# Kernel optimization log

Hardware: AMD Instinct MI355X
Metric: run time of the kernel (lower is better)

The kernel has to match this reference:

```python
import jax, jax.numpy as jnp
import numpy as np

N, E = 50000, 800000
IN_F, OUT_F, H = 128, 128, 4
D = OUT_F // H  # head dim
NEG_SLOPE = 0.2
EPS = 1e-12


def setup_inputs() -> dict:
    key = jax.random.key(0)
    ks = jax.random.split(key, 10)
    s = 1.0 / np.sqrt(IN_F)
    return {
        "x": jax.random.normal(ks[0], (N, IN_F), jnp.float32),
        "W_src": jax.random.normal(ks[1], (IN_F, H * D), jnp.float32) * s,
        "b_src": jnp.zeros((H * D,), jnp.float32),
        "W_dst": jax.random.normal(ks[2], (IN_F, H * D), jnp.float32) * s,
        "b_dst": jnp.zeros((H * D,), jnp.float32),
        "attn": jax.random.normal(ks[3], (H, D), jnp.float32) * (1.0 / np.sqrt(D)),
        "out_bias": jnp.zeros((H * D,), jnp.float32),
        "ln_w": jnp.ones((OUT_F,), jnp.float32),
        "ln_b": jnp.zeros((OUT_F,), jnp.float32),
        "src": jax.random.randint(ks[4], (E,), 0, N, jnp.int32),
        "dst": jax.random.randint(ks[5], (E,), 0, N, jnp.int32),
    }


def reference(x, W_src, b_src, W_dst, b_dst, attn, out_bias, ln_w, ln_b, src, dst):
    n = x.shape[0]
    # GATv2Conv (share_weights=False): separate source/dest projections
    fs = (x @ W_src + b_src).reshape(n, H, D)  # [N,H,D]
    fd = (x @ W_dst + b_dst).reshape(n, H, D)
    # per-edge scores: e_ij = attn . leaky_relu(fs[u] + fd[v])
    e = jax.nn.leaky_relu(fs[src] + fd[dst], NEG_SLOPE)  # [E,H,D]
    logits = jnp.einsum("ehd,hd->eh", e, attn)  # [E,H]
    # edge softmax over incoming edges of each dst node
    m = jax.ops.segment_max(logits, dst, num_segments=n)  # [N,H]
    ex = jnp.exp(logits - m[dst])
    denom = jax.ops.segment_sum(ex, dst, num_segments=n)  # [N,H]
    alpha = ex / denom[dst]  # [E,H]
    # aggregate: sum_j alpha_ij * fs[j]
    msg = alpha[:, :, None] * fs[src]  # [E,H,D]
    rst = jax.ops.segment_sum(msg, dst, num_segments=n)  # [N,H,D]
    h = rst.reshape(n, H * D) + out_bias
    # LayerNorm (biased variance, eps inside sqrt)
    u = h.mean(-1, keepdims=True)
    s = jnp.mean((h - u) ** 2, -1, keepdims=True)
    h = (h - u) / jnp.sqrt(s + EPS)
    h = ln_w * h + ln_b
    # activation = elu; dropout p=0 -> identity
    return jax.nn.elu(h)
```

## Files before the change

### kernel.cpp

```cpp
#include <hip/hip_runtime.h>
#include <hip/hip_bf16.h>

constexpr int NF = 128;

using bf16x8 = __attribute__((ext_vector_type(8))) short;
using f32x4v = __attribute__((ext_vector_type(4))) float;

__device__ __forceinline__ unsigned short f2bs(float f) {
    return __builtin_bit_cast(unsigned short, __float2bfloat16(f));
}
__device__ __forceinline__ void unpack8(float4 raw, float* a) {
    unsigned u0 = __float_as_uint(raw.x);
    unsigned u1 = __float_as_uint(raw.y);
    unsigned u2 = __float_as_uint(raw.z);
    unsigned u3 = __float_as_uint(raw.w);
    a[0] = __uint_as_float(u0 << 16);
    a[1] = __uint_as_float(u0 & 0xffff0000u);
    a[2] = __uint_as_float(u1 << 16);
    a[3] = __uint_as_float(u1 & 0xffff0000u);
    a[4] = __uint_as_float(u2 << 16);
    a[5] = __uint_as_float(u2 & 0xffff0000u);
    a[6] = __uint_as_float(u3 << 16);
    a[7] = __uint_as_float(u3 & 0xffff0000u);
}

__global__ void GraphAttnLayer_70196945486348_kernel() {}

__global__ __launch_bounds__(256) void prep_kernel(
    const float* __restrict__ Wsrc, const float* __restrict__ Wdst,
    unsigned short* __restrict__ Wb,
    int* __restrict__ state, int NSB)
{
    int i = blockIdx.x * 256 + threadIdx.x;
    if (i < NSB) state[i] = 0;
    if (i < 256 * NF) {
        int k   = i >> 8;
        int col = i & 255;
        float v = (col < 128) ? Wsrc[k * NF + col] : Wdst[k * NF + (col - 128)];
        Wb[col * NF + k] = f2bs(v);
    }
}

__global__ __launch_bounds__(256) void gemm_hist_kernel(
    const float* __restrict__ x,
    const unsigned short* __restrict__ Wb,
    const float* __restrict__ bsrc, const float* __restrict__ bdst,
    unsigned short* __restrict__ fs,
    float* __restrict__ fd,
    const int* __restrict__ dst,
    int* __restrict__ cntT,
    int N, int E, int C, int B)
{
    __shared__ int lh[256];
    const int t = threadIdx.x;
    if (blockIdx.x < C) {
        lh[t] = 0;
        __syncthreads();
        int e0 = blockIdx.x * 4096;
#pragma unroll
        for (int j = 0; j < 16; ++j) {
            int e = e0 + j * 256 + t;
            if (e < E) atomicAdd(&lh[dst[e] >> 8], 1);
        }
        __syncthreads();
        if (t < B) cntT[t * C + blockIdx.x] = lh[t];
    }

    const int lane = t & 63;
    const int wave = t >> 6;
    const int m_base = blockIdx.x * 32;
    if (m_base >= N) return;
    const int lm = lane & 15;
    const int kq = (lane >> 4) * 8;

    bf16x8 bfrag[4][4];
    float bias[4];
#pragma unroll
    for (int c = 0; c < 4; ++c) {
        int col = wave * 64 + c * 16 + lm;
        bias[c] = (col < 128) ? bsrc[col] : bdst[col - 128];
#pragma unroll
        for (int s = 0; s < 4; ++s)
            bfrag[c][s] = *(const bf16x8*)(Wb + col * NF + s * 32 + kq);
    }

    for (int r = 0; r < 2; ++r) {
        int m0 = m_base + r * 16;
        if (m0 >= N) break;
        int row = m0 + lm;
        if (row >= N) row = N - 1;
        bf16x8 afrag[4];
#pragma unroll
        for (int s = 0; s < 4; ++s) {
            const float4* xp = (const float4*)(x + (size_t)row * NF + s * 32 + kq);
            float4 xa = xp[0], xb = xp[1];
            afrag[s][0] = (short)f2bs(xa.x);
            afrag[s][1] = (short)f2bs(xa.y);
            afrag[s][2] = (short)f2bs(xa.z);
            afrag[s][3] = (short)f2bs(xa.w);
            afrag[s][4] = (short)f2bs(xb.x);
            afrag[s][5] = (short)f2bs(xb.y);
            afrag[s][6] = (short)f2bs(xb.z);
            afrag[s][7] = (short)f2bs(xb.w);
        }
#pragma unroll
        for (int c = 0; c < 4; ++c) {
            f32x4v acc = {0.f, 0.f, 0.f, 0.f};
#pragma unroll
            for (int s = 0; s < 4; ++s)
                acc = __builtin_amdgcn_mfma_f32_16x16x32_bf16(afrag[s], bfrag[c][s], acc, 0, 0, 0);
            int col = wave * 64 + c * 16 + lm;
            int cc = col & 127;
#pragma unroll
            for (int rr = 0; rr < 4; ++rr) {
                int rowd = m0 + (lane >> 4) * 4 + rr;
                if (rowd < N) {
                    float v = acc[rr] + bias[c];
                    if (col < 128) fs[(size_t)rowd * NF + cc] = f2bs(v);
                    else           fd[(size_t)rowd * NF + cc] = v;
                }
            }
        }
    }
}

__global__ __launch_bounds__(256) void scan_kernel(
    const int* __restrict__ cntT, int* __restrict__ baseBC,
    int* __restrict__ state, int M)
{
    int b = blockIdx.x, t = threadIdx.x;
    int i = b * 256 + t;
    int v = (i < M) ? cntT[i] : 0;

    __shared__ int arr[256];
    __shared__ int s_bofs;
    arr[t] = v;
    __syncthreads();
    for (int off = 1; off < 256; off <<= 1) {
        int u = (t >= off) ? arr[t - off] : 0;
        __syncthreads();
        arr[t] += u;
        __syncthreads();
    }
    int total = arr[255];

    if (t < 64) {
        if (t == 0) {
            int word = ((b == 0 ? 2 : 1) << 30) | total;
            atomicExch(&state[b], word);
        }
        int bofs = 0;
        if (b > 0) {
            int base = b;
            for (;;) {
                int j = base - 1 - t;
                int sv = 0, f = 1;
                if (j >= 0) {
                    sv = __hip_atomic_load(&state[j], __ATOMIC_RELAXED,
                                           __HIP_MEMORY_SCOPE_AGENT);
                    f = ((unsigned)sv) >> 30;
                }
                unsigned long long notready = __ballot(f == 0);
                if (notready) continue;
                unsigned long long has2 = __ballot(f == 2);
                if (has2) {
                    int k = (int)(__ffsll((unsigned long long)has2) - 1);
                    int val = (t <= k) ? (sv & 0x3FFFFFFF) : 0;
#pragma unroll
                    for (int off = 32; off; off >>= 1) val += __shfl_xor(val, off);
                    bofs += val;
                    break;
                } else {
                    int val = (j >= 0) ? (sv & 0x3FFFFFFF) : 0;
#pragma unroll
                    for (int off = 32; off; off >>= 1) val += __shfl_xor(val, off);
                    bofs += val;
                    base -= 64;
                }
            }
            if (t == 0) atomicExch(&state[b], (2 << 30) | (bofs + total));
        }
        if (t == 0) s_bofs = bofs;
    }
    __syncthreads();
    int excl = arr[t] - v + s_bofs;
    if (i < M) baseBC[i] = excl;
}

__global__ __launch_bounds__(256) void scatter_pairs_kernel(
    const int* __restrict__ dst, const int* __restrict__ src,
    const int* __restrict__ baseBC, unsigned* __restrict__ pairs,
    int E, int C, int B)
{
    __shared__ int base_lds[256];
    __shared__ int lcnt[256];
    int chunk = blockIdx.x, t = threadIdx.x;
    if (t < B) base_lds[t] = baseBC[t * C + chunk];
    lcnt[t] = 0;
    __syncthreads();
    int e0 = chunk * 4096;
#pragma unroll
    for (int j = 0; j < 16; ++j) {
        int e = e0 + j * 256 + t;
        if (e < E) {
            int d = dst[e];
            int b = d >> 8;
            int r = atomicAdd(&lcnt[b], 1);
            pairs[base_lds[b] + r] = ((unsigned)(d & 255) << 16) | (unsigned)src[e];
        }
    }
}

__global__ __launch_bounds__(256) void bucket_sort_kernel(
    const unsigned* __restrict__ pairs, const int* __restrict__ baseBC,
    int* __restrict__ rowptr, unsigned short* __restrict__ src_sorted,
    int N, int E, int C, int B)
{
    __shared__ int h[256];
    __shared__ int arr[256];
    __shared__ int cur[256];
    __shared__ unsigned short sorted[16384];
    int b = blockIdx.x, t = threadIdx.x;
    int segbase = baseBC[b * C];
    int end = (b + 1 < B) ? baseBC[(b + 1) * C] : E;
    int count = end - segbase;

    h[t] = 0;
    __syncthreads();
    for (int i = t; i < count; i += 256)
        atomicAdd(&h[pairs[segbase + i] >> 16], 1);
    __syncthreads();
    int v = h[t];
    arr[t] = v;
    __syncthreads();
    for (int off = 1; off < 256; off <<= 1) {
        int u = (t >= off) ? arr[t - off] : 0;
        __syncthreads();
        arr[t] += u;
        __syncthreads();
    }
    int excl = arr[t] - v;
    int node = b * 256 + t;
    if (node <= N) rowptr[node] = segbase + excl;
    cur[t] = excl;
    __syncthreads();
    for (int i = t; i < count; i += 256) {
        unsigned p = pairs[segbase + i];
        int r = atomicAdd(&cur[p >> 16], 1);
        sorted[r] = (unsigned short)(p & 0xFFFF);
    }
    __syncthreads();
    for (int i = t; i < count; i += 256)
        src_sorted[segbase + i] = sorted[i];
}

__global__ __launch_bounds__(256) void node_kernel(
    const float4* __restrict__ fsq,
    const int* __restrict__ rowptr, const unsigned short* __restrict__ src_sorted,
    const float4* __restrict__ attn4,
    const float4* __restrict__ obias4,
    const float4* __restrict__ lnw4,
    const float4* __restrict__ lnb4,
    float4* __restrict__ out4, int N)
{
    int lane = threadIdx.x & 63;
    int es = lane >> 4;
    int g  = lane & 15;
    int n = blockIdx.x * 4 + (threadIdx.x >> 6);
    if (n >= N) return;

    float4 fda = out4[(size_t)n * 32 + g * 2];
    float4 fdb = out4[(size_t)n * 32 + g * 2 + 1];
    float4 ava = attn4[g * 2];
    float4 avb = attn4[g * 2 + 1];
    float fd[8] = {fda.x, fda.y, fda.z, fda.w, fdb.x, fdb.y, fdb.z, fdb.w};
    float av[8] = {ava.x, ava.y, ava.z, ava.w, avb.x, avb.y, avb.z, avb.w};

    int beg = rowptr[n], end = rowptr[n + 1];
    float l = 0.f;
    float ac[8] = {0.f, 0.f, 0.f, 0.f, 0.f, 0.f, 0.f, 0.f};

    for (int j = beg; j < end; j += 4) {
        int idx = j + es;
        bool valid = idx < end;
        int s = src_sorted[valid ? idx : (end - 1)];
        float4 raw = fsq[(size_t)s * 16 + g];
        float a[8];
        unpack8(raw, a);
        float p = 0.f;
#pragma unroll
        for (int d = 0; d < 8; ++d) {
            float t = a[d] + fd[d];
            t = fmaxf(t, 0.2f * t);
            p += av[d] * t;
        }
        p += __shfl_xor(p, 1);
        p += __shfl_xor(p, 2);
        float e = valid ? __expf(p) : 0.f;
        l += e;
#pragma unroll
        for (int d = 0; d < 8; ++d) ac[d] += e * a[d];
    }

    l += __shfl_xor(l, 16);
    l += __shfl_xor(l, 32);
#pragma unroll
    for (int d = 0; d < 8; ++d) {
        ac[d] += __shfl_xor(ac[d], 16);
        ac[d] += __shfl_xor(ac[d], 32);
    }

    float rl = (l > 0.f) ? (1.f / l) : 0.f;
    float4 oba = obias4[g * 2];
    float4 obb = obias4[g * 2 + 1];
    float ob[8] = {oba.x, oba.y, oba.z, oba.w, obb.x, obb.y, obb.z, obb.w};
    float h[8];
    float s1 = 0.f, s2 = 0.f;
#pragma unroll
    for (int d = 0; d < 8; ++d) {
        h[d] = ac[d] * rl + ob[d];
        s1 += h[d];
        s2 += h[d] * h[d];
    }
    s1 += __shfl_xor(s1, 1); s2 += __shfl_xor(s2, 1);
    s1 += __shfl_xor(s1, 2); s2 += __shfl_xor(s2, 2);
    s1 += __shfl_xor(s1, 4); s2 += __shfl_xor(s2, 4);
    s1 += __shfl_xor(s1, 8); s2 += __shfl_xor(s2, 8);

    float u = s1 * (1.f / NF);
    float var = s2 * (1.f / NF) - u * u;
    float rstd = rsqrtf(fmaxf(var, 0.f) + 1e-12f);
    float4 gwa = lnw4[g * 2], gwb = lnw4[g * 2 + 1];
    float4 gba = lnb4[g * 2], gbb = lnb4[g * 2 + 1];
    float gw[8] = {gwa.x, gwa.y, gwa.z, gwa.w, gwb.x, gwb.y, gwb.z, gwb.w};
    float gb[8] = {gba.x, gba.y, gba.z, gba.w, gbb.x, gbb.y, gbb.z, gbb.w};
    float z[8];
#pragma unroll
    for (int d = 0; d < 8; ++d) {
        float y = gw[d] * ((h[d] - u) * rstd) + gb[d];
        z[d] = (y > 0.f) ? y : (__expf(y) - 1.f);
    }
    if (es == 0) {
        out4[(size_t)n * 32 + g * 2]     = make_float4(z[0], z[1], z[2], z[3]);
        out4[(size_t)n * 32 + g * 2 + 1] = make_float4(z[4], z[5], z[6], z[7]);
    }
}

extern "C" void kernel_launch(void* const* d_in, const int* in_sizes, int n_in,
                              void* d_out, int out_size, void* d_ws, size_t ws_size,
                              hipStream_t stream)
{
    const float* x    = (const float*)d_in[0];
    const float* Wsrc = (const float*)d_in[1];
    const float* bsrc = (const float*)d_in[2];
    const float* Wdst = (const float*)d_in[3];
    const float* bdst = (const float*)d_in[4];
    const float4* attn4 = (const float4*)d_in[5];
    const float4* obias4= (const float4*)d_in[6];
    const float4* lnw4  = (const float4*)d_in[7];
    const float4* lnb4  = (const float4*)d_in[8];
    const int* src = (const int*)d_in[9];
    const int* dst = (const int*)d_in[10];
    int N = in_sizes[0] / NF;
    int E = in_sizes[9];

    int C = (E + 4095) / 4096;
    int B = (N + 255) / 256;
    int M = B * C;
    int NSB = (M + 255) / 256;

    int* cntT = (int*)d_ws;
    int* baseBC = cntT + M;
    int* state = baseBC + M;
    int* rowptr = state + 256;
    unsigned* pairs = (unsigned*)(rowptr + (N + 1));
    unsigned short* srcs = (unsigned short*)(pairs + E);
    unsigned short* Wb = srcs + ((E + 1) & ~1);
    unsigned short* fs = Wb + 256 * NF;

    int NGB = (N + 31) / 32;
    if (NGB < C) NGB = C;

    prep_kernel<<<B, 256, 0, stream>>>(Wsrc, Wdst, Wb, state, NSB);
    gemm_hist_kernel<<<NGB, 256, 0, stream>>>(
        x, Wb, bsrc, bdst, fs, (float*)d_out, dst, cntT, N, E, C, B);
    scan_kernel<<<NSB, 256, 0, stream>>>(cntT, baseBC, state, M);
    scatter_pairs_kernel<<<C, 256, 0, stream>>>(dst, src, baseBC, pairs, E, C, B);
    bucket_sort_kernel<<<B, 256, 0, stream>>>(pairs, baseBC, rowptr, srcs, N, E, C, B);
    node_kernel<<<(N + 3) / 4, 256, 0, stream>>>(
        (const float4*)fs, rowptr, srcs, attn4, obias4, lnw4, lnb4,
        (float4*)d_out, N);
}
```

Before: 208.8 us.

## Pre-swizzle weight fragments and stage x tile through LDS in GEMM

The prep kernel now writes the bf16 weights in per-thread MFMA fragment order, so each GEMM thread loads its B fragments with contiguous, coalesced 16-byte reads. The GEMM block also loads its 32x128 x tile into padded shared memory with coalesced float4 reads, then builds A fragments from LDS instead of doing strided global reads per lane. This targets uncoalesced global loads in the projection GEMM, at the cost of extra shared memory, a block barrier, and scalar LDS reads.

```diff
diff --git a/kernel.cpp b/kernel.cpp
--- a/kernel.cpp
+++ b/kernel.cpp
@@ -28,22 +28,35 @@
 
 __global__ __launch_bounds__(256) void prep_kernel(
     const float* __restrict__ Wsrc, const float* __restrict__ Wdst,
-    unsigned short* __restrict__ Wb,
+    unsigned short* __restrict__ Wb2,
     int* __restrict__ state, int NSB)
 {
     int i = blockIdx.x * 256 + threadIdx.x;
     if (i < NSB) state[i] = 0;
-    if (i < 256 * NF) {
-        int k   = i >> 8;
-        int col = i & 255;
-        float v = (col < 128) ? Wsrc[k * NF + col] : Wdst[k * NF + (col - 128)];
-        Wb[col * NF + k] = f2bs(v);
+    if (i < 16 * 256) {
+        int j = i >> 8;
+        int t = i & 255;
+        int wave = t >> 6;
+        int lane = t & 63;
+        int lm = lane & 15;
+        int kq = (lane >> 4) * 8;
+        int c = j >> 2, s = j & 3;
+        int col = wave * 64 + c * 16 + lm;
+        int ks = s * 32 + kq;
+        bf16x8 frag;
+#pragma unroll
+        for (int m = 0; m < 8; ++m) {
+            float v = (col < 128) ? Wsrc[(ks + m) * NF + col]
+                                  : Wdst[(ks + m) * NF + (col - 128)];
+            frag[m] = (short)f2bs(v);
+        }
+        *(bf16x8*)(Wb2 + (size_t)i * 8) = frag;
     }
 }
 
 __global__ __launch_bounds__(256) void gemm_hist_kernel(
     const float* __restrict__ x,
-    const unsigned short* __restrict__ Wb,
+    const unsigned short* __restrict__ Wb2,
     const float* __restrict__ bsrc, const float* __restrict__ bdst,
     unsigned short* __restrict__ fs,
     float* __restrict__ fd,
@@ -52,6 +65,7 @@
     int N, int E, int C, int B)
 {
     __shared__ int lh[256];
+    __shared__ float xs[32][129];
     const int t = threadIdx.x;
     if (blockIdx.x < C) {
         lh[t] = 0;
@@ -81,27 +95,34 @@
         bias[c] = (col < 128) ? bsrc[col] : bdst[col - 128];
 #pragma unroll
         for (int s = 0; s < 4; ++s)
-            bfrag[c][s] = *(const bf16x8*)(Wb + col * NF + s * 32 + kq);
-    }
+            bfrag[c][s] = *(const bf16x8*)(Wb2 + ((size_t)((c * 4 + s) * 256 + t)) * 8);
+    }
+
+#pragma unroll
+    for (int q = 0; q < 4; ++q) {
+        int idx = q * 256 + t;
+        int row = idx >> 5;
+        int c4  = (idx & 31) * 4;
+        int grow = m_base + row;
+        if (grow >= N) grow = N - 1;
+        float4 v = *(const float4*)(x + (size_t)grow * NF + c4);
+        xs[row][c4 + 0] = v.x;
+        xs[row][c4 + 1] = v.y;
+        xs[row][c4 + 2] = v.z;
+        xs[row][c4 + 3] = v.w;
+    }
+    __syncthreads();
 
     for (int r = 0; r < 2; ++r) {
         int m0 = m_base + r * 16;
         if (m0 >= N) break;
-        int row = m0 + lm;
-        if (row >= N) row = N - 1;
         bf16x8 afrag[4];
 #pragma unroll
         for (int s = 0; s < 4; ++s) {
-            const float4* xp = (const float4*)(x + (size_t)row * NF + s * 32 + kq);
-            float4 xa = xp[0], xb = xp[1];
-            afrag[s][0] = (short)f2bs(xa.x);
-            afrag[s][1] = (short)f2bs(xa.y);
-            afrag[s][2] = (short)f2bs(xa.z);
-            afrag[s][3] = (short)f2bs(xa.w);
-            afrag[s][4] = (short)f2bs(xb.x);
-            afrag[s][5] = (short)f2bs(xb.y);
-            afrag[s][6] = (short)f2bs(xb.z);
-            afrag[s][7] = (short)f2bs(xb.w);
+            const float* xp = &xs[r * 16 + lm][s * 32 + kq];
+#pragma unroll
+            for (int j = 0; j < 8; ++j)
+                afrag[s][j] = (short)f2bs(xp[j]);
         }
 #pragma unroll
         for (int c = 0; c < 4; ++c) {
@@ -375,15 +396,15 @@
     int* rowptr = state + 256;
     unsigned* pairs = (unsigned*)(rowptr + (N + 1));
     unsigned short* srcs = (unsigned short*)(pairs + E);
-    unsigned short* Wb = srcs + ((E + 1) & ~1);
-    unsigned short* fs = Wb + 256 * NF;
+    unsigned short* Wb2 = srcs + ((E + 1) & ~1);
+    unsigned short* fs = Wb2 + 16 * 256 * 8;
 
     int NGB = (N + 31) / 32;
     if (NGB < C) NGB = C;
 
-    prep_kernel<<<B, 256, 0, stream>>>(Wsrc, Wdst, Wb, state, NSB);
+    prep_kernel<<<B, 256, 0, stream>>>(Wsrc, Wdst, Wb2, state, NSB);
     gemm_hist_kernel<<<NGB, 256, 0, stream>>>(
-        x, Wb, bsrc, bdst, fs, (float*)d_out, dst, cntT, N, E, C, B);
+        x, Wb2, bsrc, bdst, fs, (float*)d_out, dst, cntT, N, E, C, B);
     scan_kernel<<<NSB, 256, 0, stream>>>(cntT, baseBC, state, M);
     scatter_pairs_kernel<<<C, 256, 0, stream>>>(dst, src, baseBC, pairs, E, C, B);
     bucket_sort_kernel<<<B, 256, 0, stream>>>(pairs, baseBC, rowptr, srcs, N, E, C, B);
```

After: 193.7 us. -7.2%, faster.
